# Kernel tuning notes

Hardware: AMD Instinct MI355X
Metric: run time of the kernel (lower is better)

Reference implementation:

```python
import jax, jax.numpy as jnp
import numpy as np


def setup_inputs() -> dict:
    key = jax.random.key(0)
    k1, k2 = jax.random.split(key)
    B, C, N, M = 8, 3, 4096, 4096
    source_point_cloud = jax.random.normal(k1, (B, C, N), dtype=jnp.float32)
    target_point_cloud = jax.random.normal(k2, (B, C, M), dtype=jnp.float32)
    return {"source_point_cloud": source_point_cloud,
            "target_point_cloud": target_point_cloud}


def _nn_indices(source, target):
    # source: [B,3,N], target: [B,3,M]
    # squared Euclidean distance: |s|^2 + |t|^2 - 2 s.t  (monotone in true distance,
    # so argmin matches the KD-tree nearest-neighbor query)
    s2 = jnp.sum(source * source, axis=1)               # [B,N]
    t2 = jnp.sum(target * target, axis=1)               # [B,M]
    cross = jnp.einsum('bcn,bcm->bnm', source, target)  # [B,N,M]
    d2 = s2[:, :, None] + t2[:, None, :] - 2.0 * cross  # [B,N,M]
    return jnp.argmin(d2, axis=2)                       # [B,N]


def reference(source_point_cloud, target_point_cloud):
    # Per-batch: nearest target point for each source point, then mean MSE.
    idx = _nn_indices(source_point_cloud, target_point_cloud)        # [B,N]
    # gather matched target points: [B,3,N]
    matched = jnp.take_along_axis(target_point_cloud, idx[:, None, :], axis=2)
    diff = source_point_cloud - matched
    # MSELoss over the (1,3,N) batch slice -> mean over 3*N elements; one scalar per batch
    loss_per_batch = jnp.mean(diff * diff, axis=(1, 2))              # [B]
    return loss_per_batch
```

## Files before the change

### kernel.cpp

```cpp
#include <hip/hip_runtime.h>


#define B_ 8
#define N_ 4096
#define CH 4096
#define BS 12288
#define TQ 512
#define BIG 3.4e38f

__global__ __launch_bounds__(512, 8)
void nn_loss_main(const float* __restrict__ src,
                  const float* __restrict__ tgt,
                  float* __restrict__ partial) {
    __shared__ __align__(16) char smem[8 * TQ * 4];
    float4* stage = (float4*)smem;
    float*  red   = (float*)smem;

    const int tid  = threadIdx.x;
    const int blk  = blockIdx.x;
    const int b    = blk >> 6;
    const int e    = (blk >> 3) & 7;
    const int sgrp = blk & 7;
    const int ls   = tid & 63;
    const int w    = tid >> 6;

    {
        const float* tb = tgt + b * BS;
        const int m = (e << 9) + tid;
        float x = tb[m], y = tb[m + CH], z = tb[m + 2 * CH];
        stage[tid] = make_float4(x, y, z, x * x + y * y + z * z);
    }

    const float* sb = src + b * BS;
    float ax[8], ay[8], az[8];
    #pragma unroll
    for (int j = 0; j < 8; ++j) {
        int n = (sgrp << 9) + (j << 6) + ls;
        ax[j] = -2.0f * sb[n];
        ay[j] = -2.0f * sb[n + CH];
        az[j] = -2.0f * sb[n + 2 * CH];
    }

    __syncthreads();

    float best[8];
    #pragma unroll
    for (int j = 0; j < 8; ++j) best[j] = BIG;

    const float4* tp = stage + (w << 6);
    #pragma unroll 2
    for (int i = 0; i < 64; i += 2) {
        float4 t0 = tp[i];
        float4 t1 = tp[i + 1];
        #pragma unroll
        for (int j = 0; j < 8; ++j) {
            float d0 = fmaf(ax[j], t0.x, fmaf(ay[j], t0.y, fmaf(az[j], t0.z, t0.w)));
            float d1 = fmaf(ax[j], t1.x, fmaf(ay[j], t1.y, fmaf(az[j], t1.z, t1.w)));
            best[j] = fminf(fminf(best[j], d0), d1);
        }
    }

    __syncthreads();

    #pragma unroll
    for (int j = 0; j < 8; ++j) {
        float s2 = 0.25f * fmaf(ax[j], ax[j], fmaf(ay[j], ay[j], az[j] * az[j]));
        red[(w << 9) + (j << 6) + ls] = best[j] + s2;
    }

    __syncthreads();

    float mn = red[tid];
    #pragma unroll
    for (int v = 1; v < 8; ++v)
        mn = fminf(mn, red[(v << 9) + tid]);
    partial[(e << 15) + (b << 12) + (sgrp << 9) + tid] = mn;
}

__global__ __launch_bounds__(1024)
void reduce_kernel(const float* __restrict__ partial,
                   float* __restrict__ out) {
    const int b = blockIdx.x;
    const int tid = threadIdx.x;

    float acc = 0.0f;
    #pragma unroll
    for (int j = 0; j < 4; ++j) {
        int base = (b << 12) + (j << 10) + tid;
        float mn = partial[base];
        #pragma unroll
        for (int e = 1; e < 8; ++e)
            mn = fminf(mn, partial[(e << 15) + base]);
        acc += mn;
    }

    #pragma unroll
    for (int off = 32; off > 0; off >>= 1)
        acc += __shfl_down(acc, off, 64);

    __shared__ float red[16];
    if ((tid & 63) == 0) red[tid >> 6] = acc;
    __syncthreads();
    if (tid == 0) {
        float v = 0.0f;
        #pragma unroll
        for (int k = 0; k < 16; ++k) v += red[k];
        out[b] = v * (1.0f / (3.0f * (float)N_));
    }
}

extern "C" void kernel_launch(void* const* d_in, const int* in_sizes, int n_in,
                              void* d_out, int out_size, void* d_ws, size_t ws_size,
                              hipStream_t stream) {
    const float* src = (const float*)d_in[0];
    const float* tgt = (const float*)d_in[1];
    float* out = (float*)d_out;
    float* partial = (float*)d_ws;

    nn_loss_main<<<512, 512, 0, stream>>>(src, tgt, partial);
    reduce_kernel<<<B_, 1024, 0, stream>>>(partial, out);
}
```

Before: 67.09 us.

## Split targets into 16 chunks of 256 and vectorize source loads

Halves the per-block target tile from 512 to 256 points and doubles the grid to 1024 blocks, so more waves are resident to hide latency. Each thread now loads its 8 source points with float4 reads of contiguous indices, and the reduction layout in shared memory is changed to match. The final reduce kernel takes the min over 16 partials instead of 8. In exchange, source loading and the reduction happen twice as often overall, and both the partial buffer and the reduce traffic double.

New measurement: 70.43 us. 5.0% more time.

```diff
diff --git a/kernel.cpp b/kernel.cpp
--- a/kernel.cpp
+++ b/kernel.cpp
@@ -5,41 +5,47 @@
 #define N_ 4096
 #define CH 4096
 #define BS 12288
-#define TQ 512
+#define TQ 256
 #define BIG 3.4e38f
 
 __global__ __launch_bounds__(512, 8)
 void nn_loss_main(const float* __restrict__ src,
                   const float* __restrict__ tgt,
                   float* __restrict__ partial) {
-    __shared__ __align__(16) char smem[8 * TQ * 4];
+    __shared__ __align__(16) char smem[8 * 512 * 4];
     float4* stage = (float4*)smem;
     float*  red   = (float*)smem;
 
     const int tid  = threadIdx.x;
     const int blk  = blockIdx.x;
-    const int b    = blk >> 6;
-    const int e    = (blk >> 3) & 7;
+    const int b    = blk >> 7;
+    const int c    = (blk >> 3) & 15;
     const int sgrp = blk & 7;
     const int ls   = tid & 63;
     const int w    = tid >> 6;
 
-    {
+    if (tid < TQ) {
         const float* tb = tgt + b * BS;
-        const int m = (e << 9) + tid;
+        const int m = (c << 8) + tid;
         float x = tb[m], y = tb[m + CH], z = tb[m + 2 * CH];
         stage[tid] = make_float4(x, y, z, x * x + y * y + z * z);
     }
 
-    const float* sb = src + b * BS;
+    const float* sbase = src + b * BS + (sgrp << 9) + (ls << 3);
+    float4 xa = ((const float4*)sbase)[0];
+    float4 xb = ((const float4*)sbase)[1];
+    float4 ya = ((const float4*)(sbase + CH))[0];
+    float4 yb = ((const float4*)(sbase + CH))[1];
+    float4 za = ((const float4*)(sbase + 2 * CH))[0];
+    float4 zb = ((const float4*)(sbase + 2 * CH))[1];
+
     float ax[8], ay[8], az[8];
-    #pragma unroll
-    for (int j = 0; j < 8; ++j) {
-        int n = (sgrp << 9) + (j << 6) + ls;
-        ax[j] = -2.0f * sb[n];
-        ay[j] = -2.0f * sb[n + CH];
-        az[j] = -2.0f * sb[n + 2 * CH];
-    }
+    ax[0] = -2.0f * xa.x; ax[1] = -2.0f * xa.y; ax[2] = -2.0f * xa.z; ax[3] = -2.0f * xa.w;
+    ax[4] = -2.0f * xb.x; ax[5] = -2.0f * xb.y; ax[6] = -2.0f * xb.z; ax[7] = -2.0f * xb.w;
+    ay[0] = -2.0f * ya.x; ay[1] = -2.0f * ya.y; ay[2] = -2.0f * ya.z; ay[3] = -2.0f * ya.w;
+    ay[4] = -2.0f * yb.x; ay[5] = -2.0f * yb.y; ay[6] = -2.0f * yb.z; ay[7] = -2.0f * yb.w;
+    az[0] = -2.0f * za.x; az[1] = -2.0f * za.y; az[2] = -2.0f * za.z; az[3] = -2.0f * za.w;
+    az[4] = -2.0f * zb.x; az[5] = -2.0f * zb.y; az[6] = -2.0f * zb.z; az[7] = -2.0f * zb.w;
 
     __syncthreads();
 
@@ -47,9 +53,9 @@
     #pragma unroll
     for (int j = 0; j < 8; ++j) best[j] = BIG;
 
-    const float4* tp = stage + (w << 6);
-    #pragma unroll 2
-    for (int i = 0; i < 64; i += 2) {
+    const float4* tp = stage + (w << 5);
+    #pragma unroll 4
+    for (int i = 0; i < 32; i += 2) {
         float4 t0 = tp[i];
         float4 t1 = tp[i + 1];
         #pragma unroll
@@ -65,7 +71,7 @@
     #pragma unroll
     for (int j = 0; j < 8; ++j) {
         float s2 = 0.25f * fmaf(ax[j], ax[j], fmaf(ay[j], ay[j], az[j] * az[j]));
-        red[(w << 9) + (j << 6) + ls] = best[j] + s2;
+        red[(w << 9) + (ls << 3) + j] = best[j] + s2;
     }
 
     __syncthreads();
@@ -74,7 +80,7 @@
     #pragma unroll
     for (int v = 1; v < 8; ++v)
         mn = fminf(mn, red[(v << 9) + tid]);
-    partial[(e << 15) + (b << 12) + (sgrp << 9) + tid] = mn;
+    partial[(c << 15) + (b << 12) + (sgrp << 9) + tid] = mn;
 }
 
 __global__ __launch_bounds__(1024)
@@ -89,8 +95,8 @@
         int base = (b << 12) + (j << 10) + tid;
         float mn = partial[base];
         #pragma unroll
-        for (int e = 1; e < 8; ++e)
-            mn = fminf(mn, partial[(e << 15) + base]);
+        for (int c = 1; c < 16; ++c)
+            mn = fminf(mn, partial[(c << 15) + base]);
         acc += mn;
     }
 
@@ -117,6 +123,6 @@
     float* out = (float*)d_out;
     float* partial = (float*)d_ws;
 
-    nn_loss_main<<<512, 512, 0, stream>>>(src, tgt, partial);
+    nn_loss_main<<<1024, 512, 0, stream>>>(src, tgt, partial);
     reduce_kernel<<<B_, 1024, 0, stream>>>(partial, out);
 }
```
